# Kernel tuning notes

Hardware: AMD Instinct MI355X
Metric: run time of the kernel (lower is better)

## Reference

```python
import jax, jax.numpy as jnp
import numpy as np

VOCAB, D, L, H, B, S = 10000, 512, 6, 8, 32, 384
DK = D // H
DFF = 4 * D
EPS = 1e-5


def setup_inputs() -> dict:
    key = jax.random.key(0)
    ks = jax.random.split(key, 24)
    sc = 0.02
    emb = jax.random.normal(ks[0], (VOCAB, D), jnp.float32) * sc
    emb = emb.at[0].set(0.0)  # padding_idx=0
    inp = {
        'input_id': jax.random.randint(ks[1], (B, S), 0, VOCAB),
        'intensity': jax.random.uniform(ks[2], (B, 1, S), jnp.float32),
        'emb': emb,
        'iw': jax.random.normal(ks[3], (1, D), jnp.float32) * sc,
        'ib': jnp.zeros((D,), jnp.float32),
        'Wq': jax.random.normal(ks[4], (L, D, D), jnp.float32) * sc,
        'bq': jnp.zeros((L, D), jnp.float32),
        'Wk': jax.random.normal(ks[5], (L, D, D), jnp.float32) * sc,
        'bk': jnp.zeros((L, D), jnp.float32),
        'Wv': jax.random.normal(ks[6], (L, D, D), jnp.float32) * sc,
        'bv': jnp.zeros((L, D), jnp.float32),
        'Wo': jax.random.normal(ks[7], (L, D, D), jnp.float32) * sc,
        'bo': jnp.zeros((L, D), jnp.float32),
        'ln1w': jnp.ones((L, D), jnp.float32),
        'ln1b': jnp.zeros((L, D), jnp.float32),
        'ln2w': jnp.ones((L, D), jnp.float32),
        'ln2b': jnp.zeros((L, D), jnp.float32),
        'W1': jax.random.normal(ks[8], (L, D, DFF), jnp.float32) * sc,
        'b1': jnp.zeros((L, DFF), jnp.float32),
        'W2': jax.random.normal(ks[9], (L, DFF, D), jnp.float32) * sc,
        'b2': jnp.zeros((L, D), jnp.float32),
    }
    return inp


def _ln(x, w, b):
    m = jnp.mean(x, axis=-1, keepdims=True)
    v = jnp.mean((x - m) ** 2, axis=-1, keepdims=True)
    return (x - m) / jnp.sqrt(v + EPS) * w + b


def _block(x, pad_mask, Wq, bq, Wk, bk, Wv, bv, Wo, bo, ln1w, ln1b, ln2w, ln2b, W1, b1, W2, b2):
    b, s, d = x.shape
    h = _ln(x, ln1w, ln1b)
    q = (h @ Wq + bq).reshape(b, s, H, DK).transpose(0, 2, 1, 3)  # [B,H,S,DK]
    k = (h @ Wk + bk).reshape(b, s, H, DK).transpose(0, 2, 1, 3)
    v = (h @ Wv + bv).reshape(b, s, H, DK).transpose(0, 2, 1, 3)
    scores = jnp.einsum('bhqd,bhkd->bhqk', q, k) / jnp.sqrt(jnp.float32(DK))
    scores = jnp.where(pad_mask, -1e9, scores)  # mask keys at pad positions
    p = jax.nn.softmax(scores, axis=-1)
    attn = jnp.einsum('bhqk,bhkd->bhqd', p, v)
    attn = attn.transpose(0, 2, 1, 3).reshape(b, s, d)
    x = x + (attn @ Wo + bo)
    h2 = _ln(x, ln2w, ln2b)
    ffn = jax.nn.gelu(h2 @ W1 + b1, approximate=False) @ W2 + b2
    return x + ffn


def reference(input_id, intensity, emb, iw, ib, Wq, bq, Wk, bk, Wv, bv, Wo, bo,
              ln1w, ln1b, ln2w, ln2b, W1, b1, W2, b2):
    # predict() path of MSBERT (deterministic; training forward adds random masking)
    inten = jnp.swapaxes(intensity, 1, 2) @ iw + ib          # [B,S,D]
    x = emb[input_id] + inten                                 # token emb + intensity proj
    pad_mask = (input_id == 0)[:, None, None, :]              # [B,1,1,S] broadcast over queries
    for i in range(L):
        x = _block(x, pad_mask, Wq[i], bq[i], Wk[i], bk[i], Wv[i], bv[i], Wo[i], bo[i],
                   ln1w[i], ln1b[i], ln2w[i], ln2b[i], W1[i], b1[i], W2[i], b2[i])
    pool = jnp.matmul(intensity, x) / jnp.float32(intensity.shape[1])  # [B,1,D]
    return pool
```

## Files before the change

kernel.cpp:

```cpp
#include <hip/hip_runtime.h>
#include <math.h>

#define VOCAB 10000
#define D 512
#define L 6
#define H 8
#define B 32
#define S 384
#define DK 64
#define DFF 2048
#define TOK (B * S)
#define TD ((size_t)TOK * D)

typedef unsigned short u16;
using bf16x8 = __attribute__((ext_vector_type(8))) short;
using f32x4  = __attribute__((ext_vector_type(4))) float;
using u16x4  = __attribute__((ext_vector_type(4))) unsigned short;

__device__ u16   g_x[TD];
__device__ u16   g_h[TD];
__device__ u16   g_q[TD];
__device__ u16   g_k[TD];
__device__ u16   g_vt[TD];
__device__ u16   g_ffn[(size_t)TOK * DFF];
__device__ u16   g_qkvT[(size_t)L * 3 * D * D];
__device__ u16   g_woT[(size_t)L * D * D];
__device__ u16   g_w1T[(size_t)L * DFF * D];
__device__ u16   g_w2T[(size_t)L * D * DFF];
__device__ float g_bqkv[L * 3 * D];
__device__ float g_pool[B * 6 * D];

__device__ __forceinline__ u16 f2bf(float f) {
  unsigned int u = __builtin_bit_cast(unsigned int, f);
  u = (u + 0x7fffu + ((u >> 16) & 1u)) >> 16;
  return (u16)u;
}
__device__ __forceinline__ float bf2f(u16 v) {
  unsigned int u = ((unsigned int)v) << 16;
  return __builtin_bit_cast(float, u);
}

__device__ __forceinline__ void gld16(const void* g, void* l) {
  __builtin_amdgcn_global_load_lds(
      (const __attribute__((address_space(1))) unsigned int*)g,
      (__attribute__((address_space(3))) unsigned int*)l, 16, 0, 0);
}

__global__ __launch_bounds__(256) void embed_kernel(
    const int* __restrict__ ids, const float* __restrict__ inten,
    const float* __restrict__ emb, const float* __restrict__ iw,
    const float* __restrict__ ib, u16* __restrict__ x) {
  int tok = blockIdx.x;
  int t = threadIdx.x;
  int id = ids[tok];
  float it = inten[tok];
  const float* er = emb + (size_t)id * D;
  u16* xr = x + (size_t)tok * D;
  xr[t]       = f2bf(er[t] + it * iw[t] + ib[t]);
  xr[t + 256] = f2bf(er[t + 256] + it * iw[t + 256] + ib[t + 256]);
}

__global__ __launch_bounds__(256) void ln_kernel(
    const u16* __restrict__ x, const float* __restrict__ w,
    const float* __restrict__ b, u16* __restrict__ out) {
  int tok = blockIdx.x * 4 + (threadIdx.x >> 6);
  int lane = threadIdx.x & 63;
  const u16* xr = x + (size_t)tok * D + lane * 8;
  bf16x8 v8 = *(const bf16x8*)xr;
  float v[8];
  float s = 0.f, ss = 0.f;
  #pragma unroll
  for (int i = 0; i < 8; ++i) {
    v[i] = bf2f((u16)v8[i]);
    s += v[i];
    ss += v[i] * v[i];
  }
  #pragma unroll
  for (int o = 1; o < 64; o <<= 1) {
    s += __shfl_xor(s, o);
    ss += __shfl_xor(ss, o);
  }
  float mean = s * (1.0f / (float)D);
  float var = ss * (1.0f / (float)D) - mean * mean;
  float rstd = rsqrtf(var + 1e-5f);
  float4 w0 = *(const float4*)(w + lane * 8);
  float4 w1 = *(const float4*)(w + lane * 8 + 4);
  float4 b0 = *(const float4*)(b + lane * 8);
  float4 b1 = *(const float4*)(b + lane * 8 + 4);
  float wv[8] = {w0.x, w0.y, w0.z, w0.w, w1.x, w1.y, w1.z, w1.w};
  float bv[8] = {b0.x, b0.y, b0.z, b0.w, b1.x, b1.y, b1.z, b1.w};
  bf16x8 o8;
  #pragma unroll
  for (int i = 0; i < 8; ++i)
    o8[i] = (short)f2bf((v[i] - mean) * rstd * wv[i] + bv[i]);
  *(bf16x8*)(out + (size_t)tok * D + lane * 8) = o8;
}

__global__ __launch_bounds__(256) void transpose_cvt(
    const float* __restrict__ src, u16* __restrict__ dst,
    int K, int N, size_t sstride, size_t dstride) {
  __shared__ float tile[32][33];
  int n0 = blockIdx.x * 32, k0 = blockIdx.y * 32, l = blockIdx.z;
  src += (size_t)l * sstride;
  dst += (size_t)l * dstride;
  int tx = threadIdx.x & 31, ty = threadIdx.x >> 5;
  #pragma unroll
  for (int i = 0; i < 32; i += 8)
    tile[ty + i][tx] = src[(size_t)(k0 + ty + i) * N + n0 + tx];
  __syncthreads();
  #pragma unroll
  for (int i = 0; i < 32; i += 8)
    dst[(size_t)(n0 + ty + i) * K + k0 + tx] = f2bf(tile[tx][ty + i]);
}

__global__ __launch_bounds__(256) void transpose_qkvo(
    const float* __restrict__ Wq, const float* __restrict__ Wk,
    const float* __restrict__ Wv, const float* __restrict__ Wo,
    u16* __restrict__ qkvT, u16* __restrict__ woT) {
  __shared__ float tile[32][33];
  int z = blockIdx.z;
  int l = z >> 2, which = z & 3;
  const float* src = (which == 0 ? Wq : which == 1 ? Wk : which == 2 ? Wv : Wo)
                     + (size_t)l * D * D;
  u16* dst = (which < 3) ? (qkvT + (size_t)l * 3 * D * D + (size_t)which * D * D)
                         : (woT + (size_t)l * D * D);
  int n0 = blockIdx.x * 32, k0 = blockIdx.y * 32;
  int tx = threadIdx.x & 31, ty = threadIdx.x >> 5;
  #pragma unroll
  for (int i = 0; i < 32; i += 8)
    tile[ty + i][tx] = src[(size_t)(k0 + ty + i) * D + n0 + tx];
  __syncthreads();
  #pragma unroll
  for (int i = 0; i < 32; i += 8)
    dst[(size_t)(n0 + ty + i) * D + k0 + tx] = f2bf(tile[tx][ty + i]);
}

__global__ __launch_bounds__(256) void concat_bias(
    const float* __restrict__ bq, const float* __restrict__ bk,
    const float* __restrict__ bv, float* __restrict__ dst) {
  int i = blockIdx.x * 256 + threadIdx.x;
  int l = i / 1536, c = i % 1536;
  float v = (c < 512) ? bq[l * 512 + c]
          : (c < 1024) ? bk[l * 512 + c - 512]
                       : bv[l * 512 + c - 1024];
  dst[i] = v;
}

template <int EPI>
__global__ __launch_bounds__(256) void mfma_gemm(
    const u16* __restrict__ A, const u16* __restrict__ Bt,
    const float* __restrict__ bias,
    u16* __restrict__ Oq, u16* __restrict__ Ok, u16* __restrict__ Ovt,
    int M, int N, int K) {
  __shared__ u16 As[2][128 * 32];
  __shared__ u16 Bs[2][128 * 32];
  int t = threadIdx.x;
  int lane = t & 63, w = t >> 6;
  int wr = w >> 1, wc = w & 1;

  int gm = gridDim.y, gn = gridDim.x;
  int wgid = blockIdx.y * gn + blockIdx.x;
  int xcd = wgid & 7;
  int c = wgid >> 3;
  int rpx = gm >> 3;
  int cg = c / gn;
  int bm = (xcd * rpx + cg) * 128;
  int bn = (c - cg * gn) * 128;

  int l15 = lane & 15, l4 = lane >> 4;

  int gswu = ((t & 3) ^ ((t >> 3) & 3)) * 8;
  const u16* a0 = A + (size_t)(bm + (t >> 2)) * K + gswu;
  const u16* a1 = A + (size_t)(bm + 64 + (t >> 2)) * K + gswu;
  const u16* b0 = Bt + (size_t)(bn + (t >> 2)) * K + gswu;
  const u16* b1 = Bt + (size_t)(bn + 64 + (t >> 2)) * K + gswu;
  unsigned off0 = (unsigned)(t & 192) * 16u;
  unsigned off1 = off0 + 256u * 16u;
  int rxu = (l4 ^ ((l15 >> 1) & 3)) * 8;

  f32x4 acc[4][4];
  #pragma unroll
  for (int mi = 0; mi < 4; ++mi)
    #pragma unroll
    for (int nj = 0; nj < 4; ++nj)
      acc[mi][nj] = f32x4{0.f, 0.f, 0.f, 0.f};

  int nt = K >> 5;

#define STAGE_T(ti, bi) do { int k0s = (ti) * 32;            \
    gld16(a0 + k0s, (char*)As[bi] + off0);                   \
    gld16(a1 + k0s, (char*)As[bi] + off1);                   \
    gld16(b0 + k0s, (char*)Bs[bi] + off0);                   \
    gld16(b1 + k0s, (char*)Bs[bi] + off1); } while (0)

  STAGE_T(0, 0);
  STAGE_T(1, 1);

  for (int tt = 0; tt < nt; ++tt) {
    if (tt < nt - 1) asm volatile("s_waitcnt vmcnt(4)" ::: "memory");
    else             asm volatile("s_waitcnt vmcnt(0)" ::: "memory");
    __builtin_amdgcn_s_barrier();
    __builtin_amdgcn_sched_barrier(0);
    const u16* Asb = As[tt & 1];
    const u16* Bsb = Bs[tt & 1];
    bf16x8 af[4], bfr[4];
    #pragma unroll
    for (int mi = 0; mi < 4; ++mi)
      af[mi] = *(const bf16x8*)(Asb + (wr * 64 + mi * 16 + l15) * 32 + rxu);
    #pragma unroll
    for (int nj = 0; nj < 4; ++nj)
      bfr[nj] = *(const bf16x8*)(Bsb + (wc * 64 + nj * 16 + l15) * 32 + rxu);
    #pragma unroll
    for (int mi = 0; mi < 4; ++mi)
      #pragma unroll
      for (int nj = 0; nj < 4; ++nj)
        acc[mi][nj] = __builtin_amdgcn_mfma_f32_16x16x32_bf16(af[mi], bfr[nj], acc[mi][nj], 0, 0, 0);
    __builtin_amdgcn_sched_barrier(0);
    __builtin_amdgcn_s_barrier();
    if (tt + 2 < nt) STAGE_T(tt + 2, tt & 1);
  }
#undef STAGE_T

  int row00 = bm + wr * 64, col0 = bn + wc * 64;
  #pragma unroll
  for (int mi = 0; mi < 4; ++mi) {
    int rowb = row00 + mi * 16 + l4 * 4;
    #pragma unroll
    for (int nj = 0; nj < 4; ++nj) {
      int col = col0 + nj * 16 + l15;
      float bcol = bias[col];
      if (EPI == 0) {
        if (col < 512) {
          #pragma unroll
          for (int r = 0; r < 4; ++r)
            Oq[(size_t)(rowb + r) * D + col] = f2bf(acc[mi][nj][r] + bcol);
        } else if (col < 1024) {
          #pragma unroll
          for (int r = 0; r < 4; ++r)
            Ok[(size_t)(rowb + r) * D + (col - 512)] = f2bf(acc[mi][nj][r] + bcol);
        } else {
          int cv = col - 1024;
          int hh = cv >> 6, dk = cv & 63;
          int bb = rowb / S, ss = rowb - bb * S;
          u16x4 pk;
          #pragma unroll
          for (int r = 0; r < 4; ++r) pk[r] = f2bf(acc[mi][nj][r] + bcol);
          *(u16x4*)(Ovt + ((size_t)(bb * H + hh) * DK + dk) * S + ss) = pk;
        }
      } else {
        #pragma unroll
        for (int r = 0; r < 4; ++r) {
          float v = acc[mi][nj][r] + bcol;
          v = 0.5f * v * (1.0f + erff(v * 0.70710678118654752f));
          Oq[(size_t)(rowb + r) * N + col] = f2bf(v);
        }
      }
    }
  }
}

__global__ __launch_bounds__(256) void gemm64(
    const u16* __restrict__ A, const u16* __restrict__ Bt,
    const float* __restrict__ bias, u16* __restrict__ Cres,
    int M, int N, int K) {
  __shared__ u16 As[2][64 * 32];
  __shared__ u16 Bs[2][128 * 32];
  int t = threadIdx.x;
  int lane = t & 63, w = t >> 6;
  int wr = w >> 1, wc = w & 1;

  int gm = gridDim.y, gn = gridDim.x;
  int wgid = blockIdx.y * gn + blockIdx.x;
  int xcd = wgid & 7;
  int c = wgid >> 3;
  int rpx = gm >> 3;
  int cg = c / gn;
  int bm = (xcd * rpx + cg) * 64;
  int bn = (c - cg * gn) * 128;

  int l15 = lane & 15, l4 = lane >> 4;

  int arow = t >> 2, ag = t & 3;
  int aswu = (ag ^ ((arow >> 1) & 3)) * 8;
  const u16* a0 = A + (size_t)(bm + arow) * K + aswu;
  const u16* b0 = Bt + (size_t)(bn + arow) * K + aswu;
  const u16* b1 = Bt + (size_t)(bn + 64 + arow) * K + aswu;
  unsigned offA  = (unsigned)(w * 1024);
  unsigned offB0 = (unsigned)(w * 1024);
  unsigned offB1 = offB0 + 4096u;
  int rxu = (l4 ^ ((l15 >> 1) & 3)) * 8;

  f32x4 acc[2][4];
  #pragma unroll
  for (int mi = 0; mi < 2; ++mi)
    #pragma unroll
    for (int nj = 0; nj < 4; ++nj)
      acc[mi][nj] = f32x4{0.f, 0.f, 0.f, 0.f};

  int nt = K >> 5;

#define STG64(ti, bi) do { int k0s = (ti) * 32;              \
    gld16(a0 + k0s, (char*)As[bi] + offA);                   \
    gld16(b0 + k0s, (char*)Bs[bi] + offB0);                  \
    gld16(b1 + k0s, (char*)Bs[bi] + offB1); } while (0)

  STG64(0, 0);
  STG64(1, 1);

  for (int tt = 0; tt < nt; ++tt) {
    if (tt < nt - 1) asm volatile("s_waitcnt vmcnt(3)" ::: "memory");
    else             asm volatile("s_waitcnt vmcnt(0)" ::: "memory");
    __builtin_amdgcn_s_barrier();
    __builtin_amdgcn_sched_barrier(0);
    const u16* Asb = As[tt & 1];
    const u16* Bsb = Bs[tt & 1];
    bf16x8 af[2], bfr[4];
    #pragma unroll
    for (int mi = 0; mi < 2; ++mi)
      af[mi] = *(const bf16x8*)(Asb + (wr * 32 + mi * 16 + l15) * 32 + rxu);
    #pragma unroll
    for (int nj = 0; nj < 4; ++nj)
      bfr[nj] = *(const bf16x8*)(Bsb + (wc * 64 + nj * 16 + l15) * 32 + rxu);
    #pragma unroll
    for (int mi = 0; mi < 2; ++mi)
      #pragma unroll
      for (int nj = 0; nj < 4; ++nj)
        acc[mi][nj] = __builtin_amdgcn_mfma_f32_16x16x32_bf16(af[mi], bfr[nj], acc[mi][nj], 0, 0, 0);
    __builtin_amdgcn_sched_barrier(0);
    __builtin_amdgcn_s_barrier();
    if (tt + 2 < nt) STG64(tt + 2, tt & 1);
  }
#undef STG64

  int row00 = bm + wr * 32, col0 = bn + wc * 64;
  #pragma unroll
  for (int mi = 0; mi < 2; ++mi) {
    int rowb = row00 + mi * 16 + l4 * 4;
    #pragma unroll
    for (int nj = 0; nj < 4; ++nj) {
      int col = col0 + nj * 16 + l15;
      float bcol = bias[col];
      #pragma unroll
      for (int r = 0; r < 4; ++r) {
        size_t ci = (size_t)(rowb + r) * N + col;
        Cres[ci] = f2bf(bf2f(Cres[ci]) + acc[mi][nj][r] + bcol);
      }
    }
  }
}

__global__ __launch_bounds__(256) void attn_mfma(
    const u16* __restrict__ q, const u16* __restrict__ k,
    const u16* __restrict__ vt, const int* __restrict__ ids,
    u16* __restrict__ out) {
  __shared__ u16 Ks[64][72];
  __shared__ u16 Vs[64][72];
  __shared__ u16 Pt[4][32][66];
  __shared__ float Msall[S];
  int t = threadIdx.x, lane = t & 63, w = t >> 6;
  int l15 = lane & 15, l4 = lane >> 4;
  int bh = blockIdx.x;
  int b = bh >> 3, hh = bh & 7;
  int q0 = blockIdx.y * 128 + w * 32;

  for (int i = t; i < S; i += 256)
    Msall[i] = (ids[b * S + i] == 0) ? -1e9f : -8.0f;

  bf16x8 qf[2][2];
  const u16* qbase = q + (size_t)(b * S + q0) * D + hh * DK;
  #pragma unroll
  for (int mi = 0; mi < 2; ++mi)
    #pragma unroll
    for (int ks = 0; ks < 2; ++ks)
      qf[mi][ks] = *(const bf16x8*)(qbase + (size_t)(mi * 16 + l15) * D + ks * 32 + l4 * 8);

  int rr0 = t >> 3, ch0 = t & 7;
  int rr1 = (256 + t) >> 3, ch1 = t & 7;
  const size_t kbase = (size_t)(b * S) * D + hh * DK;
  const size_t vbase = (size_t)(b * H + hh) * DK * S;

  bf16x8 kr0, kr1, vr0, vr1;
  kr0 = *(const bf16x8*)(k + kbase + (size_t)rr0 * D + ch0 * 8);
  kr1 = *(const bf16x8*)(k + kbase + (size_t)rr1 * D + ch1 * 8);
  vr0 = *(const bf16x8*)(vt + vbase + (size_t)rr0 * S + 0 + ch0 * 8);
  vr1 = *(const bf16x8*)(vt + vbase + (size_t)rr1 * S + 0 + ch1 * 8);
  *(bf16x8*)(&Ks[rr0][ch0 * 8]) = kr0;
  *(bf16x8*)(&Ks[rr1][ch1 * 8]) = kr1;
  *(bf16x8*)(&Vs[rr0][ch0 * 8]) = vr0;
  *(bf16x8*)(&Vs[rr1][ch1 * 8]) = vr1;
  __syncthreads();

  float lsum_sw[2] = {0.f, 0.f};
  f32x4 accO[2][4];
  #pragma unroll
  for (int mi = 0; mi < 2; ++mi)
    #pragma unroll
    for (int nj = 0; nj < 4; ++nj)
      accO[mi][nj] = f32x4{0.f, 0.f, 0.f, 0.f};

  for (int kt = 0; kt < S; kt += 64) {
    bool more = (kt + 64) < S;
    if (more) {
      kr0 = *(const bf16x8*)(k + kbase + (size_t)(kt + 64 + rr0) * D + ch0 * 8);
      kr1 = *(const bf16x8*)(k + kbase + (size_t)(kt + 64 + rr1) * D + ch1 * 8);
      vr0 = *(const bf16x8*)(vt + vbase + (size_t)rr0 * S + kt + 64 + ch0 * 8);
      vr1 = *(const bf16x8*)(vt + vbase + (size_t)rr1 * S + kt + 64 + ch1 * 8);
    }

    f32x4 scT[4][2];
    #pragma unroll
    for (int kb = 0; kb < 4; ++kb)
      #pragma unroll
      for (int mi = 0; mi < 2; ++mi)
        scT[kb][mi] = f32x4{0.f, 0.f, 0.f, 0.f};
    __builtin_amdgcn_s_setprio(1);
    #pragma unroll
    for (int ks = 0; ks < 2; ++ks) {
      bf16x8 kf[4];
      #pragma unroll
      for (int kb = 0; kb < 4; ++kb)
        kf[kb] = *(const bf16x8*)(&Ks[kb * 16 + l15][ks * 32 + l4 * 8]);
      #pragma unroll
      for (int kb = 0; kb < 4; ++kb)
        #pragma unroll
        for (int mi = 0; mi < 2; ++mi)
          scT[kb][mi] = __builtin_amdgcn_mfma_f32_16x16x32_bf16(kf[kb], qf[mi][ks], scT[kb][mi], 0, 0, 0);
    }
    __builtin_amdgcn_s_setprio(0);

    #pragma unroll
    for (int kb = 0; kb < 4; ++kb) {
      float mvv[4];
      #pragma unroll
      for (int r = 0; r < 4; ++r)
        mvv[r] = Msall[kt + kb * 16 + l4 * 4 + r];
      #pragma unroll
      for (int mi = 0; mi < 2; ++mi) {
        u16x4 pk;
        #pragma unroll
        for (int r = 0; r < 4; ++r) {
          float p = __expf(scT[kb][mi][r] * 0.125f + mvv[r]);
          lsum_sw[mi] += p;
          pk[r] = f2bf(p);
        }
        *(u16x4*)(&Pt[w][mi * 16 + l15][kb * 16 + l4 * 4]) = pk;
      }
    }

    __builtin_amdgcn_s_setprio(1);
    #pragma unroll
    for (int ks2 = 0; ks2 < 2; ++ks2) {
      bf16x8 pf[2], vf[4];
      #pragma unroll
      for (int mi = 0; mi < 2; ++mi)
        pf[mi] = *(const bf16x8*)(&Pt[w][mi * 16 + l15][ks2 * 32 + l4 * 8]);
      #pragma unroll
      for (int nj = 0; nj < 4; ++nj)
        vf[nj] = *(const bf16x8*)(&Vs[nj * 16 + l15][ks2 * 32 + l4 * 8]);
      #pragma unroll
      for (int mi = 0; mi < 2; ++mi)
        #pragma unroll
        for (int nj = 0; nj < 4; ++nj)
          accO[mi][nj] = __builtin_amdgcn_mfma_f32_16x16x32_bf16(pf[mi], vf[nj], accO[mi][nj], 0, 0, 0);
    }
    __builtin_amdgcn_s_setprio(0);

    if (more) {
      __syncthreads();
      *(bf16x8*)(&Ks[rr0][ch0 * 8]) = kr0;
      *(bf16x8*)(&Ks[rr1][ch1 * 8]) = kr1;
      *(bf16x8*)(&Vs[rr0][ch0 * 8]) = vr0;
      *(bf16x8*)(&Vs[rr1][ch1 * 8]) = vr1;
      __syncthreads();
    }
  }

  float inv_[2][4];
  #pragma unroll
  for (int mi = 0; mi < 2; ++mi) {
    float tot = lsum_sw[mi];
    tot += __shfl_xor(tot, 16);
    tot += __shfl_xor(tot, 32);
    #pragma unroll
    for (int r = 0; r < 4; ++r)
      inv_[mi][r] = 1.0f / __shfl(tot, l4 * 4 + r);
  }

  #pragma unroll
  for (int mi = 0; mi < 2; ++mi)
    #pragma unroll
    for (int nj = 0; nj < 4; ++nj)
      #pragma unroll
      for (int r = 0; r < 4; ++r) {
        int row = b * S + q0 + mi * 16 + l4 * 4 + r;
        out[(size_t)row * D + hh * DK + nj * 16 + l15] =
            f2bf(accO[mi][nj][r] * inv_[mi][r]);
      }
}

__global__ __launch_bounds__(512) void pool_part(
    const u16* __restrict__ x, const float* __restrict__ inten,
    float* __restrict__ part) {
  int b = blockIdx.x, cchunk = blockIdx.y;
  int d = threadIdx.x;
  int s0 = cchunk * 64;
  float acc = 0.f;
  for (int s = s0; s < s0 + 64; ++s)
    acc += inten[b * S + s] * bf2f(x[((size_t)b * S + s) * D + d]);
  part[((size_t)b * 6 + cchunk) * D + d] = acc;
}
__global__ __launch_bounds__(512) void pool_reduce(
    const float* __restrict__ part, float* __restrict__ out) {
  int b = blockIdx.x, d = threadIdx.x;
  float acc = 0.f;
  #pragma unroll
  for (int c = 0; c < 6; ++c) acc += part[((size_t)b * 6 + c) * D + d];
  out[b * D + d] = acc;
}

extern "C" void kernel_launch(void* const* d_in, const int* in_sizes, int n_in,
                              void* d_out, int out_size, void* d_ws, size_t ws_size,
                              hipStream_t stream) {
  const int* input_id    = (const int*)d_in[0];
  const float* intensity = (const float*)d_in[1];
  const float* emb = (const float*)d_in[2];
  const float* iw  = (const float*)d_in[3];
  const float* ib  = (const float*)d_in[4];
  const float* Wq  = (const float*)d_in[5];
  const float* bq  = (const float*)d_in[6];
  const float* Wk  = (const float*)d_in[7];
  const float* bk  = (const float*)d_in[8];
  const float* Wv  = (const float*)d_in[9];
  const float* bv  = (const float*)d_in[10];
  const float* Wo  = (const float*)d_in[11];
  const float* bo  = (const float*)d_in[12];
  const float* ln1w = (const float*)d_in[13];
  const float* ln1b = (const float*)d_in[14];
  const float* ln2w = (const float*)d_in[15];
  const float* ln2b = (const float*)d_in[16];
  const float* W1  = (const float*)d_in[17];
  const float* b1  = (const float*)d_in[18];
  const float* W2  = (const float*)d_in[19];
  const float* b2  = (const float*)d_in[20];
  float* outp = (float*)d_out;

  float *bqkv, *poolp;
  u16 *x, *h, *q, *k, *vt, *ffn, *qkvT, *woT, *w1T, *w2T;
  { void* p; hipGetSymbolAddress(&p, HIP_SYMBOL(g_x));    x    = (u16*)p; }
  { void* p; hipGetSymbolAddress(&p, HIP_SYMBOL(g_h));    h    = (u16*)p; }
  { void* p; hipGetSymbolAddress(&p, HIP_SYMBOL(g_q));    q    = (u16*)p; }
  { void* p; hipGetSymbolAddress(&p, HIP_SYMBOL(g_k));    k    = (u16*)p; }
  { void* p; hipGetSymbolAddress(&p, HIP_SYMBOL(g_vt));   vt   = (u16*)p; }
  { void* p; hipGetSymbolAddress(&p, HIP_SYMBOL(g_ffn));  ffn  = (u16*)p; }
  { void* p; hipGetSymbolAddress(&p, HIP_SYMBOL(g_qkvT)); qkvT = (u16*)p; }
  { void* p; hipGetSymbolAddress(&p, HIP_SYMBOL(g_woT));  woT  = (u16*)p; }
  { void* p; hipGetSymbolAddress(&p, HIP_SYMBOL(g_w1T));  w1T  = (u16*)p; }
  { void* p; hipGetSymbolAddress(&p, HIP_SYMBOL(g_w2T));  w2T  = (u16*)p; }
  { void* p; hipGetSymbolAddress(&p, HIP_SYMBOL(g_bqkv)); bqkv = (float*)p; }
  { void* p; hipGetSymbolAddress(&p, HIP_SYMBOL(g_pool)); poolp = (float*)p; }

  dim3 t256(256);
  transpose_qkvo<<<dim3(16, 16, 4 * L), t256, 0, stream>>>(Wq, Wk, Wv, Wo, qkvT, woT);
  transpose_cvt<<<dim3(64, 16, L), t256, 0, stream>>>(W1, w1T, D, DFF, (size_t)D * DFF, (size_t)D * DFF);
  transpose_cvt<<<dim3(16, 64, L), t256, 0, stream>>>(W2, w2T, DFF, D, (size_t)DFF * D, (size_t)DFF * D);
  concat_bias<<<L * 3 * D / 256, t256, 0, stream>>>(bq, bk, bv, bqkv);

  embed_kernel<<<TOK, t256, 0, stream>>>(input_id, intensity, emb, iw, ib, x);

  for (int l = 0; l < L; ++l) {
    const u16* qkvT_l = qkvT + (size_t)l * 3 * D * D;
    const u16* woT_l  = woT + (size_t)l * D * D;
    const u16* w1T_l  = w1T + (size_t)l * D * DFF;
    const u16* w2T_l  = w2T + (size_t)l * DFF * D;

    ln_kernel<<<TOK / 4, t256, 0, stream>>>(x, ln1w + (size_t)l * D, ln1b + (size_t)l * D, h);
    mfma_gemm<0><<<dim3(12, 96), t256, 0, stream>>>(h, qkvT_l, bqkv + l * 3 * D,
                                                    q, k, vt, TOK, 3 * D, D);
    attn_mfma<<<dim3(B * H, S / 128), t256, 0, stream>>>(q, k, vt, input_id, h);
    gemm64<<<dim3(4, 192), t256, 0, stream>>>(h, woT_l, bo + (size_t)l * D,
                                              x, TOK, D, D);
    ln_kernel<<<TOK / 4, t256, 0, stream>>>(x, ln2w + (size_t)l * D, ln2b + (size_t)l * D, h);
    mfma_gemm<2><<<dim3(16, 96), t256, 0, stream>>>(h, w1T_l, b1 + (size_t)l * DFF,
                                                    ffn, nullptr, nullptr, TOK, DFF, D);
    gemm64<<<dim3(4, 192), t256, 0, stream>>>(ffn, w2T_l, b2 + (size_t)l * D,
                                              x, TOK, D, DFF);
  }

  pool_part<<<dim3(B, 6), dim3(512), 0, stream>>>(x, intensity, poolp);
  pool_reduce<<<B, dim3(512), 0, stream>>>(poolp, outp);
}
```

Before: 1.157 ms.

## Restructure GEMM double-buffer pipeline to one barrier per k-tile

Both GEMM kernels change from a two-tiles-ahead prefetch with two barriers per iteration to a one-tile-ahead prefetch. The next tile's loads are issued before this tile's MFMAs, then a full vmcnt(0) wait and a single barrier close the iteration. This halves the barrier count per k-step, at the cost of less prefetch depth and more exposed global load latency. Correctness relies on the barrier at the end of each iteration so the buffer being overwritten is no longer being read.

```diff
diff --git a/kernel.cpp b/kernel.cpp
--- a/kernel.cpp
+++ b/kernel.cpp
@@ -194,15 +194,14 @@
     gld16(b1 + k0s, (char*)Bs[bi] + off1); } while (0)
 
   STAGE_T(0, 0);
-  STAGE_T(1, 1);
+  asm volatile("s_waitcnt vmcnt(0)" ::: "memory");
+  __builtin_amdgcn_s_barrier();
 
   for (int tt = 0; tt < nt; ++tt) {
-    if (tt < nt - 1) asm volatile("s_waitcnt vmcnt(4)" ::: "memory");
-    else             asm volatile("s_waitcnt vmcnt(0)" ::: "memory");
-    __builtin_amdgcn_s_barrier();
-    __builtin_amdgcn_sched_barrier(0);
-    const u16* Asb = As[tt & 1];
-    const u16* Bsb = Bs[tt & 1];
+    int cur = tt & 1;
+    if (tt + 1 < nt) STAGE_T(tt + 1, cur ^ 1);
+    const u16* Asb = As[cur];
+    const u16* Bsb = Bs[cur];
     bf16x8 af[4], bfr[4];
     #pragma unroll
     for (int mi = 0; mi < 4; ++mi)
@@ -216,8 +215,10 @@
       for (int nj = 0; nj < 4; ++nj)
         acc[mi][nj] = __builtin_amdgcn_mfma_f32_16x16x32_bf16(af[mi], bfr[nj], acc[mi][nj], 0, 0, 0);
     __builtin_amdgcn_sched_barrier(0);
-    __builtin_amdgcn_s_barrier();
-    if (tt + 2 < nt) STAGE_T(tt + 2, tt & 1);
+    if (tt + 1 < nt) {
+      asm volatile("s_waitcnt vmcnt(0)" ::: "memory");
+      __builtin_amdgcn_s_barrier();
+    }
   }
 #undef STAGE_T
 
@@ -305,15 +306,14 @@
     gld16(b1 + k0s, (char*)Bs[bi] + offB1); } while (0)
 
   STG64(0, 0);
-  STG64(1, 1);
+  asm volatile("s_waitcnt vmcnt(0)" ::: "memory");
+  __builtin_amdgcn_s_barrier();
 
   for (int tt = 0; tt < nt; ++tt) {
-    if (tt < nt - 1) asm volatile("s_waitcnt vmcnt(3)" ::: "memory");
-    else             asm volatile("s_waitcnt vmcnt(0)" ::: "memory");
-    __builtin_amdgcn_s_barrier();
-    __builtin_amdgcn_sched_barrier(0);
-    const u16* Asb = As[tt & 1];
-    const u16* Bsb = Bs[tt & 1];
+    int cur = tt & 1;
+    if (tt + 1 < nt) STG64(tt + 1, cur ^ 1);
+    const u16* Asb = As[cur];
+    const u16* Bsb = Bs[cur];
     bf16x8 af[2], bfr[4];
     #pragma unroll
     for (int mi = 0; mi < 2; ++mi)
@@ -327,8 +327,10 @@
       for (int nj = 0; nj < 4; ++nj)
         acc[mi][nj] = __builtin_amdgcn_mfma_f32_16x16x32_bf16(af[mi], bfr[nj], acc[mi][nj], 0, 0, 0);
     __builtin_amdgcn_sched_barrier(0);
-    __builtin_amdgcn_s_barrier();
-    if (tt + 2 < nt) STG64(tt + 2, tt & 1);
+    if (tt + 1 < nt) {
+      asm volatile("s_waitcnt vmcnt(0)" ::: "memory");
+      __builtin_amdgcn_s_barrier();
+    }
   }
 #undef STG64
 
```

Result: slower. 1.414 ms (+22.2%).
